# Kernel optimization log

Measured on AMD Instinct MI355X. Metric: run time of the kernel, lower is better.

## Reference

```python
import jax, jax.numpy as jnp
import numpy as np

NB, NA, NC, NH, NW = 64, 5, 20, 64, 64
MAX_BBOX = 50
ANCHORS = jnp.array([[1.3221, 1.73145], [3.19275, 4.00944], [5.05587, 8.09892],
                     [9.47112, 4.84053], [11.2364, 10.0071]], dtype=jnp.float32)
COORD_SCALE = 1.0
NOOBJ_SCALE = 1.0
OBJ_SCALE = 1.0
CLASS_SCALE = 1.0
SIL_THRESH = 0.6


def iou_xywh(b1, b2):
    # center-format IoU, matching marvis bbox_ious(x1y1x2y2=False)
    x1, y1, w1, h1 = b1[..., 0], b1[..., 1], b1[..., 2], b1[..., 3]
    x2, y2, w2, h2 = b2[..., 0], b2[..., 1], b2[..., 2], b2[..., 3]
    Mx = jnp.maximum(x1 + w1 * 0.5, x2 + w2 * 0.5)
    mx = jnp.minimum(x1 - w1 * 0.5, x2 - w2 * 0.5)
    My = jnp.maximum(y1 + h1 * 0.5, y2 + h2 * 0.5)
    my = jnp.minimum(y1 - h1 * 0.5, y2 - h2 * 0.5)
    cw = w1 + w2 - (Mx - mx)
    ch = h1 + h2 - (My - my)
    carea = jnp.where((cw <= 0) | (ch <= 0), 0.0, cw * ch)
    uarea = w1 * h1 + w2 * h2 - carea
    return carea / uarea


def setup_inputs():
    key = jax.random.key(0)
    ko, kc, kx, ky, kw, kh = jax.random.split(key, 6)
    output = jax.random.normal(ko, (NB, NA * (5 + NC), NH, NW), dtype=jnp.float32) * 0.5
    cls = jax.random.randint(kc, (NB, MAX_BBOX), 0, NC).astype(jnp.float32)
    bx = jax.random.uniform(kx, (NB, MAX_BBOX), minval=0.05, maxval=0.95)
    by = jax.random.uniform(ky, (NB, MAX_BBOX), minval=0.05, maxval=0.95)
    bw = jax.random.uniform(kw, (NB, MAX_BBOX), minval=0.02, maxval=0.30)
    bh = jax.random.uniform(kh, (NB, MAX_BBOX), minval=0.02, maxval=0.30)
    target = jnp.stack([cls, bx, by, bw, bh], axis=-1).reshape(NB, MAX_BBOX * 5)
    return {"output": output, "target": target}


def _forward(output, target):
    nB, nH, nW = output.shape[0], output.shape[2], output.shape[3]
    nA, nC = NA, NC
    nTot = nB * nA * nH * nW
    out = output.reshape(nB, nA, 5 + nC, nH, nW)
    x = jax.nn.sigmoid(out[:, :, 0])
    y = jax.nn.sigmoid(out[:, :, 1])
    w = jnp.exp(out[:, :, 2])
    h = jnp.exp(out[:, :, 3])
    conf = jax.nn.sigmoid(out[:, :, 4])
    # class logits laid out exactly as torch: [nB*nA*nH*nW, nC]
    cls_logits = out[:, :, 5:].reshape(nB * nA, nC, nH * nW).transpose(0, 2, 1).reshape(nTot, nC)

    grid_x = jnp.arange(nW, dtype=jnp.float32)
    grid_y = jnp.arange(nH, dtype=jnp.float32)
    pred = jnp.stack([
        x + grid_x[None, None, None, :],
        y + grid_y[None, None, :, None],
        w * ANCHORS[None, :, 0, None, None],
        h * ANCHORS[None, :, 1, None, None],
    ], axis=-1)  # [nB, nA, nH, nW, 4] in grid units
    pred = jax.lax.stop_gradient(pred)  # torch builds pred_boxes from .data

    # ---------------- build_targets, vectorized ----------------
    tgt = target.reshape(nB, MAX_BBOX, 5)
    # loop breaks at first x==0 -> prefix validity
    valid = jnp.cumprod((tgt[:, :, 1] != 0).astype(jnp.int32), axis=1).astype(bool)
    scale = jnp.array([nW, nH, nW, nH], dtype=jnp.float32)
    gt = tgt[:, :, 1:5] * scale  # [nB, 50, 4] (gx, gy, gw, gh)

    # part 1: silence conf_mask where any gt IoU > sil_thresh
    ious = iou_xywh(gt[:, :, None, None, None, :], pred[:, None])  # [nB,50,nA,nH,nW]
    ious = jnp.where(valid[:, :, None, None, None], ious, 0.0)
    conf_mask = jnp.where(ious.max(axis=1) > SIL_THRESH, 0.0, NOOBJ_SCALE)  # [nB,nA,nH,nW]

    # part 2: best anchor per gt box (shape-only IoU at origin; anchor_step==2)
    gt0 = jnp.concatenate([jnp.zeros_like(gt[:, :, :2]), gt[:, :, 2:]], axis=-1)
    anc0 = jnp.concatenate([jnp.zeros_like(ANCHORS), ANCHORS], axis=-1)  # [nA,4]
    a_iou = iou_xywh(anc0[None, None], gt0[:, :, None, :])  # [nB,50,nA]
    best_n = jnp.argmax(a_iou, axis=-1)  # first max, matching strict > in torch loop
    gi = gt[:, :, 0].astype(jnp.int32)
    gj = gt[:, :, 1].astype(jnp.int32)
    b_idx = jnp.broadcast_to(jnp.arange(nB)[:, None], (nB, MAX_BBOX))
    flat = ((b_idx * nA + best_n) * nH + gj) * nW + gi  # [nB,50]
    flat_s = jnp.where(valid, flat, nTot).ravel()  # invalid boxes -> dummy slot

    def scatter(base_flat, vals):
        padded = jnp.concatenate([base_flat, jnp.zeros((1,), base_flat.dtype)])
        return padded.at[flat_s].set(vals.ravel())[:nTot]

    zeros_f = jnp.zeros((nTot,), jnp.float32)
    ones_bt = jnp.ones((nB, MAX_BBOX), jnp.float32)
    coord_mask = scatter(zeros_f, ones_bt)
    conf_mask = scatter(conf_mask.ravel(), jnp.full((nB, MAX_BBOX), OBJ_SCALE, jnp.float32))
    cls_mask = scatter(zeros_f, ones_bt)
    tx = scatter(zeros_f, gt[:, :, 0] - gi.astype(jnp.float32))
    ty = scatter(zeros_f, gt[:, :, 1] - gj.astype(jnp.float32))
    tw = scatter(zeros_f, gt[:, :, 2] / ANCHORS[best_n, 0])
    th = scatter(zeros_f, gt[:, :, 3] / ANCHORS[best_n, 1])
    pb = pred.reshape(nTot, 4)[flat]  # gather pred box at assigned cell, [nB,50,4]
    tconf = scatter(zeros_f, iou_xywh(gt, pb))
    tcls = scatter(zeros_f, tgt[:, :, 0])

    shape4 = (nB, nA, nH, nW)
    coord_mask = coord_mask.reshape(shape4)
    conf_mask = jnp.sqrt(conf_mask.reshape(shape4))  # marvis: conf_mask.sqrt()
    tx, ty = tx.reshape(shape4), ty.reshape(shape4)
    tw, th = tw.reshape(shape4), th.reshape(shape4)
    tconf = tconf.reshape(shape4)

    # ---------------- losses ----------------
    loss_x = COORD_SCALE * 0.5 * jnp.sum(((x - tx) * coord_mask) ** 2)
    loss_y = COORD_SCALE * 0.5 * jnp.sum(((y - ty) * coord_mask) ** 2)
    loss_w = COORD_SCALE * 0.5 * jnp.sum(((w - tw) * coord_mask) ** 2)
    loss_h = COORD_SCALE * 0.5 * jnp.sum(((h - th) * coord_mask) ** 2)
    loss_conf = 0.5 * jnp.sum(((conf - tconf) * conf_mask) ** 2)
    logp = jax.nn.log_softmax(cls_logits, axis=-1)  # [nTot, nC]
    labels = tcls.astype(jnp.int32)
    ce = -jnp.take_along_axis(logp, labels[:, None], axis=1)[:, 0]
    loss_cls = CLASS_SCALE * jnp.sum(ce * cls_mask)
    return loss_x + loss_y + loss_w + loss_h + loss_conf + loss_cls


def reference(output, target):
    return _forward(output, target)
```

## Files before the change

kernel.cpp:

```cpp
#include <hip/hip_runtime.h>
#include <cstddef>

#define NB 64
#define NA 5
#define NC 20
#define NH 64
#define NW 64
#define MAXB 50
#define HWSZ (NH * NW)
#define CELLS 5
#define CELLS_PER_BLK (256 * CELLS)
#define NABLK 64
#define NBBLK 1024
#define NPART (NABLK + NBBLK)

__constant__ float c_aw[NA] = {1.3221f, 3.19275f, 5.05587f, 9.47112f, 11.2364f};
__constant__ float c_ah[NA] = {1.73145f, 4.00944f, 8.09892f, 4.84053f, 10.0071f};

__device__ __forceinline__ float sigmoidf_(float v) {
    return 1.f / (1.f + __expf(-v));
}

__global__ __launch_bounds__(256, 4) void region_loss_main(const float* __restrict__ out,
                                                           const float* __restrict__ tgt,
                                                           float* __restrict__ partials) {
    const int bid = blockIdx.x;
    const int t = threadIdx.x;

    __shared__ __align__(16) float sbox[MAXB][8];
    __shared__ float s_cls[MAXB], s_gx[MAXB], s_gy[MAXB], s_gw[MAXB], s_gh[MAXB];
    __shared__ int s_flat[MAXB], s_bestn[MAXB];
    __shared__ int s_nv;
    __shared__ float sred[4];

    if (bid < NABLK) {
        const int b = bid;
        if (t < 64) {
            float xv = (t < MAXB) ? tgt[(size_t)b * (MAXB * 5) + t * 5 + 1] : 0.f;
            unsigned long long mk = __ballot(xv != 0.f);
            if (t == 0) {
                unsigned long long inv = (~mk) & ((1ull << MAXB) - 1ull);
                s_nv = inv ? (__ffsll(inv) - 1) : MAXB;
            }
        }
        if (t < MAXB) {
            const float* tp = tgt + (size_t)b * (MAXB * 5) + t * 5;
            s_cls[t] = tp[0];
            s_gx[t] = tp[1] * NW; s_gy[t] = tp[2] * NH;
            s_gw[t] = tp[3] * NW; s_gh[t] = tp[4] * NH;
        }
        __syncthreads();
        const int nv = s_nv;

        if (t < MAXB) {
            if (t < nv) {
                float gw = s_gw[t], gh = s_gh[t];
                float best = -1.f; int bn = 0;
                for (int a = 0; a < NA; ++a) {
                    float ca = fminf(c_aw[a], gw) * fminf(c_ah[a], gh);
                    float ua = c_aw[a] * c_ah[a] + gw * gh - ca;
                    float iou = ca / ua;
                    if (iou > best) { best = iou; bn = a; }
                }
                int gi = (int)s_gx[t], gj = (int)s_gy[t];
                s_bestn[t] = bn;
                s_flat[t] = (bn * NH + gj) * NW + gi;
            } else {
                s_flat[t] = -1 - t;
            }
        }
        __syncthreads();

        float loss = 0.f;
        if (t < nv) {
            bool winner = true;
            const int myf = s_flat[t];
            for (int t2 = t + 1; t2 < nv; ++t2) winner = winner && (s_flat[t2] != myf);
            if (winner) {
                const int a = s_bestn[t];
                const int gi = myf & (NW - 1);
                const int gj = (myf >> 6) & (NH - 1);
                const size_t base = (((size_t)b * NA + a) * 25) * HWSZ + gj * NW + gi;
                float x = sigmoidf_(out[base]);
                float y = sigmoidf_(out[base + HWSZ]);
                float w = __expf(out[base + 2 * HWSZ]);
                float h = __expf(out[base + 3 * HWSZ]);
                float conf = sigmoidf_(out[base + 4 * HWSZ]);

                float gx = s_gx[t], gy = s_gy[t], gw = s_gw[t], gh = s_gh[t];
                float tx = gx - (float)gi, ty = gy - (float)gj;
                float tw = gw / c_aw[a], th = gh / c_ah[a];
                float dx = x - tx, dy = y - ty, dw = w - tw, dh = h - th;
                loss += 0.5f * (dx * dx + dy * dy + dw * dw + dh * dh);

                float px = x + (float)gi, py = y + (float)gj;
                float pw = w * c_aw[a], ph = h * c_ah[a];
                float pxlo = px - 0.5f * pw, pxhi = px + 0.5f * pw;
                float pylo = py - 0.5f * ph, pyhi = py + 0.5f * ph;
                float parea = pw * ph;

                {
                    float cw  = fminf(pxhi, gx + 0.5f * gw) - fmaxf(pxlo, gx - 0.5f * gw);
                    float chh = fminf(pyhi, gy + 0.5f * gh) - fmaxf(pylo, gy - 0.5f * gh);
                    float ca  = fmaxf(cw, 0.f) * fmaxf(chh, 0.f);
                    float ua  = parea + gw * gh - ca;
                    float tconf = ca / ua;
                    float mm = -1e30f;
                    for (int t2 = 0; t2 < nv; ++t2) {
                        float gw2 = s_gw[t2], gh2 = s_gh[t2];
                        float cw2 = fminf(pxhi, s_gx[t2] + 0.5f * gw2) -
                                    fmaxf(pxlo, s_gx[t2] - 0.5f * gw2);
                        float ch2 = fminf(pyhi, s_gy[t2] + 0.5f * gh2) -
                                    fmaxf(pylo, s_gy[t2] - 0.5f * gh2);
                        float ca2 = fmaxf(cw2, 0.f) * fmaxf(ch2, 0.f);
                        mm = fmaxf(mm, ca2 - 0.375f * gw2 * gh2);
                    }
                    bool sil = mm > 0.375f * parea;
                    float base_c = sil ? 0.f : 0.5f * conf * conf;
                    float dc = conf - tconf;
                    loss += 0.5f * dc * dc - base_c;
                }

                {
                    const int lab = (int)s_cls[t];
                    float mmax = -1e30f, llab = 0.f;
                    for (int c = 0; c < NC; ++c) {
                        float l = out[base + (size_t)(5 + c) * HWSZ];
                        mmax = fmaxf(mmax, l);
                        if (c == lab) llab = l;
                    }
                    float se = 0.f;
                    for (int c = 0; c < NC; ++c)
                        se += __expf(out[base + (size_t)(5 + c) * HWSZ] - mmax);
                    loss += -(llab - mmax - logf(se));
                }
            }
        }
        if (t < 64) {
            for (int off = 32; off; off >>= 1) loss += __shfl_down(loss, off, 64);
            if (t == 0) partials[bid] = loss;
        }
        return;
    }

    const int g = bid - NABLK;
    const int b = g >> 4;
    const int cell0 = g * CELLS_PER_BLK;

    if (t < 64) {
        float xv = (t < MAXB) ? tgt[(size_t)b * (MAXB * 5) + t * 5 + 1] : 0.f;
        unsigned long long mk = __ballot(xv != 0.f);
        unsigned long long inv = (~mk) & ((1ull << MAXB) - 1ull);
        int nv = inv ? (__ffsll(inv) - 1) : MAXB;
        if (t < MAXB) {
            bool val = t < nv;
            const float* tp = tgt + (size_t)b * (MAXB * 5) + t * 5;
            float gx = tp[1] * (float)NW, gy = tp[2] * (float)NH;
            float gw = tp[3] * (float)NW, gh = tp[4] * (float)NH;
            sbox[t][0] = val ? gx - 0.5f * gw : 0.f;
            sbox[t][1] = val ? gx + 0.5f * gw : 0.f;
            sbox[t][2] = val ? gy - 0.5f * gh : 0.f;
            sbox[t][3] = val ? gy + 0.5f * gh : 0.f;
            sbox[t][4] = val ? 0.375f * gw * gh : 1e30f;
            sbox[t][5] = gy;
            sbox[t][6] = val ? gh : -1e9f;
        }
    }

    float pxlo[CELLS], pxhi[CELLS], pylo[CELLS], pyhi[CELLS];
    float m[CELLS], rhs[CELLS], hc[CELLS], fjh[CELLS];
    const float fi = (float)(t & 63);
#pragma unroll
    for (int cc = 0; cc < CELLS; ++cc) {
        const int cell = cell0 + cc * 256;
        const int ba = cell >> 12;
        const int a = ba - b * NA;
        const int hw = (cell & 4095) + t;
        const float fj = (float)(hw >> 6);
        const float aw = c_aw[a], ah = c_ah[a];
        const float* p = out + (size_t)ba * (25 * HWSZ) + hw;
        float px = sigmoidf_(p[0]) + fi;
        float py = sigmoidf_(p[HWSZ]) + fj;
        float pw = __expf(p[2 * HWSZ]) * aw;
        float ph = __expf(p[3 * HWSZ]) * ah;
        float cf = sigmoidf_(p[4 * HWSZ]);
        pxlo[cc] = px - 0.5f * pw; pxhi[cc] = px + 0.5f * pw;
        pylo[cc] = py - 0.5f * ph; pyhi[cc] = py + 0.5f * ph;
        rhs[cc] = 0.375f * pw * ph;
        hc[cc]  = 0.5f * cf * cf;
        m[cc]   = -1e30f;
        fjh[cc] = fj + 0.5f;
    }
    __syncthreads();

    const int lane = t & 63;
    const int li = (lane < MAXB) ? lane : 0;
    const float ls_gy = sbox[li][5];
    const float ls_thr = fmaf(0.7334f, sbox[li][6], 0.51f);
    const bool lval = lane < MAXB;

    unsigned long long msk[CELLS];
    unsigned long long u = 0ull;
#pragma unroll
    for (int cc = 0; cc < CELLS; ++cc) {
        bool p = lval && (fabsf(fjh[cc] - ls_gy) < ls_thr);
        msk[cc] = __ballot(p);
        u |= msk[cc];
    }

    if (u) {
        int bx = __ffsll(u) - 1;
        u &= u - 1;
        float4 bb = *reinterpret_cast<const float4*>(&sbox[bx][0]);
        float s2 = sbox[bx][4];
        for (;;) {
            const bool more = (u != 0ull);
            int nx = 0;
            float4 nb = bb; float ns = s2;
            if (more) {
                nx = __ffsll(u) - 1;
                u &= u - 1;
                nb = *reinterpret_cast<const float4*>(&sbox[nx][0]);
                ns = sbox[nx][4];
            }
#pragma unroll
            for (int cc = 0; cc < CELLS; ++cc) {
                if ((msk[cc] >> bx) & 1ull) {
                    float cw = fminf(pxhi[cc], bb.y) - fmaxf(pxlo[cc], bb.x);
                    float ch = fminf(pyhi[cc], bb.w) - fmaxf(pylo[cc], bb.z);
                    m[cc] = fmaxf(m[cc], fmaf(fmaxf(cw, 0.f), fmaxf(ch, 0.f), -s2));
                }
            }
            if (!more) break;
            bx = nx; bb = nb; s2 = ns;
        }
    }

    float v = 0.f;
#pragma unroll
    for (int cc = 0; cc < CELLS; ++cc) v += (m[cc] > rhs[cc]) ? 0.f : hc[cc];

    for (int off = 32; off; off >>= 1) v += __shfl_down(v, off, 64);
    if ((t & 63) == 0) sred[t >> 6] = v;
    __syncthreads();
    if (t == 0) partials[bid] = sred[0] + sred[1] + sred[2] + sred[3];
}

__global__ __launch_bounds__(256) void reduce_kernel(const float* __restrict__ partials,
                                                     float* __restrict__ outp) {
    float v = 0.f;
    for (int idx = threadIdx.x; idx < NPART; idx += 256) v += partials[idx];
    for (int off = 32; off; off >>= 1) v += __shfl_down(v, off, 64);
    __shared__ float s[4];
    if ((threadIdx.x & 63) == 0) s[threadIdx.x >> 6] = v;
    __syncthreads();
    if (threadIdx.x == 0) outp[0] = s[0] + s[1] + s[2] + s[3];
}

extern "C" void kernel_launch(void* const* d_in, const int* in_sizes, int n_in,
                              void* d_out, int out_size, void* d_ws, size_t ws_size,
                              hipStream_t stream) {
    const float* out_t = (const float*)d_in[0];
    const float* tgt   = (const float*)d_in[1];
    float* loss = (float*)d_out;
    float* partials = (float*)d_ws;

    region_loss_main<<<NPART, 256, 0, stream>>>(out_t, tgt, partials);
    reduce_kernel<<<1, 256, 0, stream>>>(partials, loss);
}
```

Baseline: 25.94 us.

## Remap noobj IoU blocks to 4 contiguous cells per thread with float4 loads

Each thread now handles four horizontally adjacent cells loaded with float4 vector loads, instead of five cells strided by 256. The block count grows to 1280, so each block covers a quarter of one anchor plane. The per-cell row-band ballot masks are replaced by a single per-wave mask: a row window around the wave's mid-row with a widened threshold, plus a new area-ratio prefilter that uses the stored gt area. This is meant to cut ballot and bit-test overhead and to improve memory coalescing. The cost is evaluating every surviving box against all four cells, and the conservativeness of the area-ratio bounds has to hold for correctness.

```diff
diff --git a/kernel.cpp b/kernel.cpp
--- a/kernel.cpp
+++ b/kernel.cpp
@@ -8,10 +8,8 @@
 #define NW 64
 #define MAXB 50
 #define HWSZ (NH * NW)
-#define CELLS 5
-#define CELLS_PER_BLK (256 * CELLS)
 #define NABLK 64
-#define NBBLK 1024
+#define NBBLK 1280
 #define NPART (NABLK + NBBLK)
 
 __constant__ float c_aw[NA] = {1.3221f, 3.19275f, 5.05587f, 9.47112f, 11.2364f};
@@ -144,8 +142,11 @@
     }
 
     const int g = bid - NABLK;
-    const int b = g >> 4;
-    const int cell0 = g * CELLS_PER_BLK;
+    const int b = g / 20;
+    const int ba = g >> 2;
+    const int a = ba - b * NA;
+    const int hw = ((g & 3) << 10) + (t << 2);
+    const int jrow = hw >> 6;
 
     if (t < 64) {
         float xv = (t < MAXB) ? tgt[(size_t)b * (MAXB * 5) + t * 5 + 1] : 0.f;
@@ -164,49 +165,55 @@
             sbox[t][4] = val ? 0.375f * gw * gh : 1e30f;
             sbox[t][5] = gy;
             sbox[t][6] = val ? gh : -1e9f;
-        }
-    }
-
-    float pxlo[CELLS], pxhi[CELLS], pylo[CELLS], pyhi[CELLS];
-    float m[CELLS], rhs[CELLS], hc[CELLS], fjh[CELLS];
-    const float fi = (float)(t & 63);
+            sbox[t][7] = val ? gw * gh : 0.f;
+        }
+    }
+
+    const float* p = out + (size_t)ba * (25 * HWSZ) + hw;
+    const float4 vx = *reinterpret_cast<const float4*>(p);
+    const float4 vy = *reinterpret_cast<const float4*>(p + HWSZ);
+    const float4 vw = *reinterpret_cast<const float4*>(p + 2 * HWSZ);
+    const float4 vh = *reinterpret_cast<const float4*>(p + 3 * HWSZ);
+    const float4 vc = *reinterpret_cast<const float4*>(p + 4 * HWSZ);
+
+    const float aw = c_aw[a], ah = c_ah[a];
+    const float fj = (float)jrow;
+    const float fi0 = (float)(hw & 63);
+
+    float pxlo[4], pxhi[4], pylo[4], pyhi[4], m4[4], rhs[4], hc[4];
+    {
+        const float xs[4] = {vx.x, vx.y, vx.z, vx.w};
+        const float ys[4] = {vy.x, vy.y, vy.z, vy.w};
+        const float ws[4] = {vw.x, vw.y, vw.z, vw.w};
+        const float hs[4] = {vh.x, vh.y, vh.z, vh.w};
+        const float cs[4] = {vc.x, vc.y, vc.z, vc.w};
 #pragma unroll
-    for (int cc = 0; cc < CELLS; ++cc) {
-        const int cell = cell0 + cc * 256;
-        const int ba = cell >> 12;
-        const int a = ba - b * NA;
-        const int hw = (cell & 4095) + t;
-        const float fj = (float)(hw >> 6);
-        const float aw = c_aw[a], ah = c_ah[a];
-        const float* p = out + (size_t)ba * (25 * HWSZ) + hw;
-        float px = sigmoidf_(p[0]) + fi;
-        float py = sigmoidf_(p[HWSZ]) + fj;
-        float pw = __expf(p[2 * HWSZ]) * aw;
-        float ph = __expf(p[3 * HWSZ]) * ah;
-        float cf = sigmoidf_(p[4 * HWSZ]);
-        pxlo[cc] = px - 0.5f * pw; pxhi[cc] = px + 0.5f * pw;
-        pylo[cc] = py - 0.5f * ph; pyhi[cc] = py + 0.5f * ph;
-        rhs[cc] = 0.375f * pw * ph;
-        hc[cc]  = 0.5f * cf * cf;
-        m[cc]   = -1e30f;
-        fjh[cc] = fj + 0.5f;
+        for (int k = 0; k < 4; ++k) {
+            float px = sigmoidf_(xs[k]) + fi0 + (float)k;
+            float py = sigmoidf_(ys[k]) + fj;
+            float pw = __expf(ws[k]) * aw;
+            float ph = __expf(hs[k]) * ah;
+            float cf = sigmoidf_(cs[k]);
+            pxlo[k] = px - 0.5f * pw; pxhi[k] = px + 0.5f * pw;
+            pylo[k] = py - 0.5f * ph; pyhi[k] = py + 0.5f * ph;
+            rhs[k] = 0.375f * pw * ph;
+            hc[k]  = 0.5f * cf * cf;
+            m4[k]  = -1e30f;
+        }
     }
     __syncthreads();
 
     const int lane = t & 63;
     const int li = (lane < MAXB) ? lane : 0;
     const float ls_gy = sbox[li][5];
-    const float ls_thr = fmaf(0.7334f, sbox[li][6], 0.51f);
-    const bool lval = lane < MAXB;
-
-    unsigned long long msk[CELLS];
-    unsigned long long u = 0ull;
-#pragma unroll
-    for (int cc = 0; cc < CELLS; ++cc) {
-        bool p = lval && (fabsf(fjh[cc] - ls_gy) < ls_thr);
-        msk[cc] = __ballot(p);
-        u |= msk[cc];
-    }
+    const float ls_thr = fmaf(0.7334f, sbox[li][6], 2.01f);
+    const float ls_ga = sbox[li][7];
+    const float A = aw * ah;
+    const float midj = (float)(((g & 3) << 4) + ((t >> 6) << 2)) + 2.0f;
+    bool keep = (lane < MAXB) &&
+                (fabsf(midj - ls_gy) < ls_thr) &&
+                (A >= 0.0505f * ls_ga) && (A <= 19.8f * ls_ga);
+    unsigned long long u = __ballot(keep);
 
     if (u) {
         int bx = __ffsll(u) - 1;
@@ -215,30 +222,27 @@
         float s2 = sbox[bx][4];
         for (;;) {
             const bool more = (u != 0ull);
-            int nx = 0;
             float4 nb = bb; float ns = s2;
             if (more) {
-                nx = __ffsll(u) - 1;
+                int nx = __ffsll(u) - 1;
                 u &= u - 1;
                 nb = *reinterpret_cast<const float4*>(&sbox[nx][0]);
                 ns = sbox[nx][4];
             }
 #pragma unroll
-            for (int cc = 0; cc < CELLS; ++cc) {
-                if ((msk[cc] >> bx) & 1ull) {
-                    float cw = fminf(pxhi[cc], bb.y) - fmaxf(pxlo[cc], bb.x);
-                    float ch = fminf(pyhi[cc], bb.w) - fmaxf(pylo[cc], bb.z);
-                    m[cc] = fmaxf(m[cc], fmaf(fmaxf(cw, 0.f), fmaxf(ch, 0.f), -s2));
-                }
+            for (int k = 0; k < 4; ++k) {
+                float cw = fminf(pxhi[k], bb.y) - fmaxf(pxlo[k], bb.x);
+                float ch = fminf(pyhi[k], bb.w) - fmaxf(pylo[k], bb.z);
+                m4[k] = fmaxf(m4[k], fmaf(fmaxf(cw, 0.f), fmaxf(ch, 0.f), -s2));
             }
             if (!more) break;
-            bx = nx; bb = nb; s2 = ns;
+            bb = nb; s2 = ns;
         }
     }
 
     float v = 0.f;
 #pragma unroll
-    for (int cc = 0; cc < CELLS; ++cc) v += (m[cc] > rhs[cc]) ? 0.f : hc[cc];
+    for (int k = 0; k < 4; ++k) v += (m4[k] > rhs[k]) ? 0.f : hc[k];
 
     for (int off = 32; off; off >>= 1) v += __shfl_down(v, off, 64);
     if ((t & 63) == 0) sred[t >> 6] = v;
```

New measurement: 26.26 us. About the same (+1.3%).
